# Kernel optimization log

Hardware: AMD Instinct MI355X
Metric: run time of the kernel (lower is better)

## Reference

```python
import jax, jax.numpy as jnp
import numpy as np

B, S, H, E, V, NSTEPS = 8, 128, 512, 512, 32000, 8


def setup_inputs() -> dict:
    key = jax.random.key(0)
    ks = jax.random.split(key, 24)

    def lin(k, fi, fo):
        return (jax.random.normal(k, (fi, fo), jnp.float32) / np.sqrt(fi).astype(np.float32))

    return {
        "input_ids": jax.random.randint(ks[0], (B, S), 0, V),
        "tree_ids": jax.random.randint(ks[1], (B, NSTEPS, 3, S), 0, S),
        "emb": jax.random.normal(ks[2], (V, E), jnp.float32) * 0.02,
        "W_ioux": lin(ks[3], E, 3 * H),
        "W_iouh_r": lin(ks[4], H, 3 * H),
        "b_iouh_r": jnp.zeros((3 * H,), jnp.float32),
        "W_iouh_l": lin(ks[5], H, 3 * H),
        "b_iouh_l": jnp.zeros((3 * H,), jnp.float32),
        "W_fx": lin(ks[6], E, H),
        "W_fh0": lin(ks[7], H, H),
        "b_fh0": jnp.zeros((H,), jnp.float32),
        "W_fh1": lin(ks[8], H, H),
        "b_fh1": jnp.zeros((H,), jnp.float32),
        "W_fh2": lin(ks[9], H, H),
        "b_fh2": jnp.zeros((H,), jnp.float32),
        "W_fh3": lin(ks[10], H, H),
        "b_fh3": jnp.zeros((H,), jnp.float32),
    }


def _scatter_rows(vals, idx):
    # out[b, idx[b, j], k] += vals[b, j, k]  (torch scatter_add_ along dim 1)
    return jax.vmap(lambda v, i: jnp.zeros_like(v).at[i].add(v))(vals, idx)


def _gather_rows(vals, idx):
    # out[b, j, k] = vals[b, idx[b, j], k]  (torch gather along dim 1)
    return jnp.take_along_axis(vals, idx[:, :, None], axis=1)


def _masked_scatter(dest, mask_rows, src):
    # Exact torch masked_scatter_ semantics: flatten mask/src, fill True slots
    # with consecutive elements of flattened src.
    m = jnp.broadcast_to(mask_rows[:, :, None], dest.shape).reshape(-1)
    pos = jnp.clip(jnp.cumsum(m) - 1, 0, None)
    out = jnp.where(m, src.reshape(-1)[pos], dest.reshape(-1))
    return out.reshape(dest.shape)


def reference(input_ids, tree_ids, emb, W_ioux, W_iouh_r, b_iouh_r, W_iouh_l,
              b_iouh_l, W_fx, W_fh0, b_fh0, W_fh1, b_fh1, W_fh2, b_fh2,
              W_fh3, b_fh3):
    x = emb[input_ids]                      # [B, S, E]
    Hs = W_fx.shape[1]
    iou_x = x @ W_ioux                      # [B, S, 3H], loop-invariant
    fx_x = x @ W_fx                         # [B, S, H],  loop-invariant
    h0 = jnp.zeros(x.shape[:2] + (Hs,), x.dtype)
    c0 = jnp.zeros_like(h0)
    steps = jnp.transpose(tree_ids, (1, 0, 2, 3))  # [n_steps, B, 3, S]

    def step(carry, t):
        h, c = carry
        idx_d, idx_r, idx_l = t[:, 0], t[:, 1], t[:, 2]
        iou_hr = h @ W_iouh_r + b_iouh_r
        iou_hl = h @ W_iouh_l + b_iouh_l
        # torch scatter_add_ with an index of width H into a 3H buffer only
        # touches the first H channels -- replicate that exactly.
        scat = _scatter_rows(iou_hr[..., :Hs], idx_r) + _scatter_rows(iou_hl[..., :Hs], idx_l)
        iou = iou_x.at[..., :Hs].add(scat)
        i, o, u = jnp.split(iou, 3, axis=-1)
        i, o, u = jax.nn.sigmoid(i), jax.nn.sigmoid(o), jnp.tanh(u)
        # fh0 and fh1 share idx_r, fh2 and fh3 share idx_l -> fold linearly.
        fh_r = h @ (W_fh0 + W_fh1) + (b_fh0 + b_fh1)
        fh_l = h @ (W_fh2 + W_fh3) + (b_fh2 + b_fh3)
        f = jax.nn.sigmoid(_gather_rows(fx_x, idx_d)
                           + _gather_rows(fh_r, idx_r)
                           + _gather_rows(fh_l, idx_l))
        fc = f * c
        c_full = i * u + _scatter_rows(fc, idx_d)
        h_full = o * jnp.tanh(c_full)
        mask = idx_d != 0
        h_new = _masked_scatter(h, mask, h_full)
        c_new = _masked_scatter(c, mask, c_full)
        return (h_new, c_new), None

    (h, c), _ = jax.lax.scan(step, (h0, c0), steps)
    return h
```

## Files before the change

kernel.cpp:

```cpp
#include <hip/hip_runtime.h>
#include <hip/hip_bf16.h>

#define B_ 8
#define S_ 128
#define H_ 512
#define E_ 512
#define NST 8
#define R_ 1024
#define N2 2048
#define KD 512
#define LDA 72
#define NBLK 512
#define GRP 64

typedef __hip_bfloat16 bf16;
typedef __attribute__((ext_vector_type(8))) short v8s;
typedef __attribute__((ext_vector_type(4))) float v4f;
typedef unsigned long long u64;

__device__ __forceinline__ float sigm(float x){ return 1.0f/(1.0f + expf(-x)); }
__device__ __forceinline__ float load_in(const void* p, long long i, int isb){
    return isb ? __bfloat162float(((const bf16*)p)[i]) : ((const float*)p)[i];
}
__device__ __forceinline__ int idx_read(const int* p, int j, int is64){
    return is64 ? p[2*j] : p[j];
}
__device__ __forceinline__ unsigned short f2b(float v){
    bf16 b = __float2bfloat16(v);
    return *(unsigned short*)&b;
}

__device__ __forceinline__ float2 vload2(const float* p){
    union { u64 u; float2 f; } c;
    c.u = __hip_atomic_load((const u64*)p, __ATOMIC_RELAXED, __HIP_MEMORY_SCOPE_AGENT);
    return c.f;
}
__device__ __forceinline__ void vstore2(float* p, float2 v){
    union { float2 f; u64 u; } c; c.f = v;
    __hip_atomic_store((u64*)p, c.u, __ATOMIC_RELAXED, __HIP_MEMORY_SCOPE_AGENT);
}
__device__ __forceinline__ void vstore1(float* p, float v){
    __hip_atomic_store(p, v, __ATOMIC_RELAXED, __HIP_MEMORY_SCOPE_AGENT);
}
__device__ __forceinline__ void vstore_hb2(unsigned short* p, unsigned short a, unsigned short b){
    unsigned int u = (unsigned)a | ((unsigned)b << 16);
    __hip_atomic_store((unsigned int*)p, u, __ATOMIC_RELAXED, __HIP_MEMORY_SCOPE_AGENT);
}
__device__ __forceinline__ v8s vload16(const unsigned short* p){
    union { u64 u[2]; v8s v; } c;
    c.u[0] = __hip_atomic_load((const u64*)p,     __ATOMIC_RELAXED, __HIP_MEMORY_SCOPE_AGENT);
    c.u[1] = __hip_atomic_load(((const u64*)p)+1, __ATOMIC_RELAXED, __HIP_MEMORY_SCOPE_AGENT);
    return c.v;
}

__device__ __forceinline__ void gsync(int* bar, int gen){
    __syncthreads();
    if (threadIdx.x == 0){
        int g = blockIdx.x >> 6;
        int* ga = bar + 64*(1+g);
        int* gd = bar + 64*(9+g);
        int old = __hip_atomic_fetch_add(ga, 1, __ATOMIC_RELAXED, __HIP_MEMORY_SCOPE_AGENT);
        if (old + 1 == GRP*gen){
            __hip_atomic_fetch_add(bar, GRP, __ATOMIC_RELAXED, __HIP_MEMORY_SCOPE_AGENT);
            while (__hip_atomic_load(bar, __ATOMIC_RELAXED, __HIP_MEMORY_SCOPE_AGENT) < NBLK*gen)
                __builtin_amdgcn_s_sleep(4);
            __hip_atomic_fetch_add(gd, 1, __ATOMIC_RELAXED, __HIP_MEMORY_SCOPE_AGENT);
        } else {
            while (__hip_atomic_load(gd, __ATOMIC_RELAXED, __HIP_MEMORY_SCOPE_AGENT) < gen)
                __builtin_amdgcn_s_sleep(4);
        }
    }
    __syncthreads();
}

__global__ void probe_all(const void* t0, const void* t1, const void* t2, const void* t3,
                          const void* t4, const void* t5, const void* t6, const void* t7,
                          const void* t8, const void* t9, const void* t10, const void* t11,
                          const void* t12, const void* t13, const void* t14,
                          const int* __restrict__ ids, const int* __restrict__ tree,
                          int* __restrict__ flags){
    const void* ts[15] = {t0,t1,t2,t3,t4,t5,t6,t7,t8,t9,t10,t11,t12,t13,t14};
    int bid = blockIdx.x, t = threadIdx.x;
    int bad = 0;
    if (bid < 15){
        if (t < 512){
            unsigned short u = ((const unsigned short*)ts[bid])[t];
            bad = (((u >> 7) & 0xFF) >= 140);
        }
    } else {
        const int* p = (bid == 15) ? ids : tree;
        int n = (bid == 15) ? 1024 : 2048;
        for (int j = t; j < n; j += 1024)
            if (j & 1) bad |= (p[j] != 0);
    }
    unsigned long long bl = __ballot(bad);
    __shared__ int acc[16];
    if ((t & 63) == 0) acc[t >> 6] = (bl != 0ull) ? 1 : 0;
    __syncthreads();
    if (t == 0){
        int any = 0;
        for (int w = 0; w < 16; ++w) any |= acc[w];
        flags[(bid < 15) ? bid : (16 + bid - 15)] = any ? 0 : 1;
    }
}

#define NB2 320
#define GS2 (NB2*512)
__global__ __launch_bounds__(512)
void rank_pack(const void* __restrict__ Wioux, const void* __restrict__ Wfx,
               const void* __restrict__ Wr, const void* __restrict__ Wl,
               const void* __restrict__ W0, const void* __restrict__ W1,
               const void* __restrict__ W2, const void* __restrict__ W3,
               const void* __restrict__ br, const void* __restrict__ bl,
               const void* __restrict__ b0, const void* __restrict__ b1,
               const void* __restrict__ b2, const void* __restrict__ b3,
               const int* __restrict__ ids, const void* __restrict__ emb,
               const int* __restrict__ tree,
               unsigned short* __restrict__ WxT, unsigned short* __restrict__ WcatT,
               float* __restrict__ bcat, unsigned short* __restrict__ xb,
               float* __restrict__ h0,
               int* __restrict__ msk, int* __restrict__ rnk, int* __restrict__ cnt,
               const int* __restrict__ flags, int* __restrict__ bar){
    int bid = blockIdx.x, tid = threadIdx.x;
    int is64 = flags[17];
    if (bid == 0){
        for (int i = tid; i < 64*17; i += 512) bar[i] = 0;
    }
    if (bid < 8){
        int st = bid;
        for (int c = tid; c < R_; c += 512){
            cnt[(0*NST + st)*R_ + c] = 0;
            cnt[(1*NST + st)*R_ + c] = 0;
            cnt[(2*NST + st)*R_ + c] = 0;
        }
        __syncthreads();
        __shared__ int wt[8];
        int runbase = 0;
        for (int ch = 0; ch < 2; ++ch){
            int t = ch*512 + tid;
            int b = t >> 7, s = t & 127;
            int base = (b*NST + st)*3*S_;
            int d0 = idx_read(tree, base + s, is64);
            int rd = (b<<7) + d0;
            int rr = (b<<7) + idx_read(tree, base + S_ + s, is64);
            int rl = (b<<7) + idx_read(tree, base + 2*S_ + s, is64);
            int m = (d0 != 0) ? 1 : 0;
            unsigned long long bal = __ballot(m);
            int lane = tid & 63, wv = tid >> 6;
            if (lane == 0) wt[wv] = __popcll(bal);
            __syncthreads();
            int bp = runbase, tot = 0;
            for (int w = 0; w < wv; ++w) bp += wt[w];
            for (int w = 0; w < 8; ++w) tot += wt[w];
            int rank = bp + __popcll(bal & ((1ull << lane) - 1ull));
            msk[st*R_ + t] = m;
            rnk[st*R_ + t] = m ? rank : 0;
            atomicAdd(&cnt[(0*NST + st)*R_ + rr], 1);
            atomicAdd(&cnt[(1*NST + st)*R_ + rl], 1);
            atomicAdd(&cnt[(2*NST + st)*R_ + rd], 1);
            runbase += tot;
            __syncthreads();
        }
    }
    int gt = bid*512 + tid;
    {
        int f_wx = flags[1], f_wf = flags[6];
        for (int u = gt; u < 131072; u += GS2){
            int n = u >> 6, k0 = (u & 63)*8;
            unsigned short tmp[8];
            #pragma unroll
            for (int i = 0; i < 8; ++i){
                float v = (n < 1536) ? load_in(Wioux, (long long)(k0+i)*1536 + n, f_wx)
                                     : load_in(Wfx,   (long long)(k0+i)*512 + (n-1536), f_wf);
                tmp[i] = f2b(v);
            }
            *(v8s*)&WxT[(size_t)n*KD + k0] = *(v8s*)tmp;
        }
    }
    {
        int fWr=flags[2], fWl=flags[4], fW0=flags[7], fW1=flags[9], fW2=flags[11], fW3=flags[13];
        for (int u = gt; u < 131072; u += GS2){
            int n = u >> 6, k0 = (u & 63)*8;
            unsigned short tmp[8];
            #pragma unroll
            for (int i = 0; i < 8; ++i){
                long long k = k0 + i;
                float v;
                if      (n <  512) v = load_in(Wr, k*1536 + n, fWr);
                else if (n < 1024) v = load_in(Wl, k*1536 + (n-512), fWl);
                else if (n < 1536) { int c = n-1024; v = load_in(W0, k*512+c, fW0) + load_in(W1, k*512+c, fW1); }
                else               { int c = n-1536; v = load_in(W2, k*512+c, fW2) + load_in(W3, k*512+c, fW3); }
                tmp[i] = f2b(v);
            }
            *(v8s*)&WcatT[(size_t)n*KD + k0] = *(v8s*)tmp;
        }
    }
    {
        int fbr=flags[3], fbl=flags[5], fb0=flags[8], fb1=flags[10], fb2=flags[12], fb3=flags[14];
        for (int n = gt; n < 2048; n += GS2){
            float v;
            if      (n <  512) v = load_in(br, n, fbr);
            else if (n < 1024) v = load_in(bl, n-512, fbl);
            else if (n < 1536) v = load_in(b0, n-1024, fb0) + load_in(b1, n-1024, fb1);
            else               v = load_in(b2, n-1536, fb2) + load_in(b3, n-1536, fb3);
            bcat[n] = v;
        }
    }
    {
        int f_emb = flags[0], i64i = flags[16];
        for (int u = gt; u < 65536; u += GS2){
            int r = u >> 6, c0 = (u & 63)*8;
            long long base = (long long)idx_read(ids, r, i64i)*E_ + c0;
            unsigned short tmp[8];
            #pragma unroll
            for (int i = 0; i < 8; ++i) tmp[i] = f2b(load_in(emb, base + i, f_emb));
            *(v8s*)&xb[(size_t)r*KD + c0] = *(v8s*)tmp;
        }
    }
    for (int u = gt; u < 262144; u += GS2)
        ((float4*)h0)[u] = make_float4(0.f,0.f,0.f,0.f);
}

__global__ void csr_scan(const int* __restrict__ cnt, int* __restrict__ off,
                         int* __restrict__ cur){
    int st = blockIdx.x, a = blockIdx.y;
    int t = threadIdx.x;
    int base = (a*NST + st)*R_;
    __shared__ int sh[R_];
    int v = cnt[base + t];
    sh[t] = v;
    __syncthreads();
    for (int d = 1; d < R_; d <<= 1){
        int x = (t >= d) ? sh[t - d] : 0;
        __syncthreads();
        sh[t] += x;
        __syncthreads();
    }
    int excl = sh[t] - v;
    off[base + t] = excl;
    cur[base + t] = excl;
}

__global__ __launch_bounds__(512)
void csr_fill(const int* __restrict__ tree, int* __restrict__ cur,
              int* __restrict__ ent, const int* __restrict__ flags){
    int is64 = flags[17];
    int st = blockIdx.x;
    for (int ch = 0; ch < 2; ++ch){
        int t = ch*512 + threadIdx.x;
        int b = t >> 7, s = t & 127;
        int base = (b*NST + st)*3*S_;
        int rd = (b<<7) + idx_read(tree, base + s, is64);
        int rr = (b<<7) + idx_read(tree, base + S_ + s, is64);
        int rl = (b<<7) + idx_read(tree, base + 2*S_ + s, is64);
        int p0 = atomicAdd(&cur[(0*NST + st)*R_ + rr], 1);
        ent[(0*NST + st)*R_ + p0] = t;
        int p1 = atomicAdd(&cur[(1*NST + st)*R_ + rl], 1);
        ent[(1*NST + st)*R_ + p1] = t;
        int p2 = atomicAdd(&cur[(2*NST + st)*R_ + rd], 1);
        ent[(2*NST + st)*R_ + p2] = t | (rr << 10) | (rl << 20);
    }
}

__device__ __forceinline__ void gemm_phase(const unsigned short* __restrict__ A,
               const unsigned short* __restrict__ BT,
               const float* __restrict__ bias,
               float* __restrict__ C,
               short* __restrict__ As, short* __restrict__ Bs)
{
    int bid = blockIdx.x;
    int bn = (bid & 7)*4 + ((bid >> 3) & 3);
    int bm = bid >> 5;
    int tid = threadIdx.x;
    int lane = tid & 63, wave = tid >> 6;
    int wm = wave & 1, wn = wave >> 1;
    int lm = lane & 15, quad = lane >> 4;
    v4f acc[2][2];
    #pragma unroll
    for (int i=0;i<2;++i)
        #pragma unroll
        for (int j=0;j<2;++j) acc[i][j] = (v4f)0.0f;

    int srow = tid >> 3, sg = (tid & 7)*8;
    const unsigned short* Ab = A  + (size_t)(bm*64)*KD;
    const unsigned short* Bb = BT + (size_t)(bn*64)*KD;
    v8s pa[2], pb[2];
    #pragma unroll
    for (int j=0;j<2;++j){
        pa[j] = vload16(Ab + (size_t)(j*32+srow)*KD + sg);
        pb[j] = *(const v8s*)(Bb + (size_t)(j*32+srow)*KD + sg);
    }
    for (int k0 = 0; k0 < KD; k0 += 64){
        #pragma unroll
        for (int j=0;j<2;++j){
            *(v8s*)&As[(j*32+srow)*LDA + sg] = pa[j];
            *(v8s*)&Bs[(j*32+srow)*LDA + sg] = pb[j];
        }
        __syncthreads();
        int k1 = k0 + 64;
        if (k1 < KD){
            #pragma unroll
            for (int j=0;j<2;++j){
                pa[j] = vload16(Ab + (size_t)(j*32+srow)*KD + k1 + sg);
                pb[j] = *(const v8s*)(Bb + (size_t)(j*32+srow)*KD + k1 + sg);
            }
        }
        #pragma unroll
        for (int kk = 0; kk < 64; kk += 32){
            v8s af[2], bf[2];
            #pragma unroll
            for (int i=0;i<2;++i){
                af[i] = *(const v8s*)&As[(wm*32 + i*16 + lm)*LDA + kk + quad*8];
                bf[i] = *(const v8s*)&Bs[(wn*32 + i*16 + lm)*LDA + kk + quad*8];
            }
            #pragma unroll
            for (int i=0;i<2;++i)
                #pragma unroll
                for (int j=0;j<2;++j)
                    acc[i][j] = __builtin_amdgcn_mfma_f32_16x16x32_bf16(af[i], bf[j], acc[i][j], 0, 0, 0);
        }
        __syncthreads();
    }
    #pragma unroll
    for (int j=0;j<2;++j){
        int n = bn*64 + wn*32 + j*16 + lm;
        float bv = bias ? bias[n] : 0.0f;
        #pragma unroll
        for (int i=0;i<2;++i){
            int m0 = bm*64 + wm*32 + i*16 + quad*4;
            #pragma unroll
            for (int rg = 0; rg < 4; ++rg)
                vstore1(&C[(size_t)(m0+rg)*N2 + n], acc[i][j][rg] + bv);
        }
    }
}

__device__ __forceinline__ void epi_phase(const float* __restrict__ XO,
              const float* __restrict__ T, int tstr,
              const float* __restrict__ hc, const float* __restrict__ cc,
              float* __restrict__ hn, float* __restrict__ cn,
              unsigned short* __restrict__ hb, float* __restrict__ out,
              const int* __restrict__ msk, const int* __restrict__ rnk,
              const int* __restrict__ cnt, const int* __restrict__ off,
              const int* __restrict__ ent, int st, int last)
{
    int tid = threadIdx.x;
    int c0 = tid*2;
    #pragma unroll
    for (int rr2 = 0; rr2 < 2; ++rr2){
        int r = blockIdx.x*2 + rr2;
        if (!msk[st*R_ + r]){
            float2 hv = vload2(&hc[(size_t)r*H_ + c0]);
            if (last){
                out[(size_t)r*H_ + c0]     = hv.x;
                out[(size_t)r*H_ + c0 + 1] = hv.y;
            } else {
                vstore2(&hn[(size_t)r*H_ + c0], hv);
                float2 cv = vload2(&cc[(size_t)r*H_ + c0]);
                vstore2(&cn[(size_t)r*H_ + c0], cv);
                vstore_hb2(&hb[(size_t)r*KD + c0], f2b(hv.x), f2b(hv.y));
            }
            continue;
        }
        int j = rnk[st*R_ + r];
        int bR = off[(0*NST+st)*R_ + j], dR = cnt[(0*NST+st)*R_ + j];
        int bL = off[(1*NST+st)*R_ + j], dL = cnt[(1*NST+st)*R_ + j];
        int bD = off[(2*NST+st)*R_ + j], dD = cnt[(2*NST+st)*R_ + j];
        const int* eR = ent + (0*NST+st)*R_ + bR;
        const int* eL = ent + (1*NST+st)*R_ + bL;
        const int* eD = ent + (2*NST+st)*R_ + bD;
        const float* xo = XO + (size_t)j*N2;
        float scv0 = 0.f, scv1 = 0.f;
        for (int e = 0; e < dR; ++e){
            float2 t = vload2(&T[(size_t)eR[e]*tstr + c0]);
            scv0 += t.x; scv1 += t.y;
        }
        for (int e = 0; e < dL; ++e){
            float2 t = vload2(&T[(size_t)eL[e]*tstr + 512 + c0]);
            scv0 += t.x; scv1 += t.y;
        }
        float2 fx = vload2(&xo[1536 + c0]);
        float csc0 = 0.f, csc1 = 0.f;
        for (int e = 0; e < dD; ++e){
            int pk = eD[e];
            int s  = pk & 1023, ra = (pk >> 10) & 1023, rb = (pk >> 20) & 1023;
            float2 ta = vload2(&T[(size_t)ra*tstr + 1024 + c0]);
            float2 tb = vload2(&T[(size_t)rb*tstr + 1536 + c0]);
            float2 cv = vload2(&cc[(size_t)s*H_ + c0]);
            float f0 = sigm(fx.x + ta.x + tb.x);
            float f1 = sigm(fx.y + ta.y + tb.y);
            csc0 += f0 * cv.x;
            csc1 += f1 * cv.y;
        }
        float2 xi = vload2(&xo[c0]);
        float2 xq = vload2(&xo[512 + c0]);
        float2 xu = vload2(&xo[1024 + c0]);
        float ig0 = sigm(xi.x + scv0), ig1 = sigm(xi.y + scv1);
        float og0 = sigm(xq.x), og1 = sigm(xq.y);
        float ug0 = tanhf(xu.x), ug1 = tanhf(xu.y);
        float cf0 = ig0*ug0 + csc0, cf1 = ig1*ug1 + csc1;
        float hf0 = og0 * tanhf(cf0), hf1 = og1 * tanhf(cf1);
        if (last){
            out[(size_t)r*H_ + c0]     = hf0;
            out[(size_t)r*H_ + c0 + 1] = hf1;
        } else {
            vstore2(&hn[(size_t)r*H_ + c0], make_float2(hf0, hf1));
            vstore2(&cn[(size_t)r*H_ + c0], make_float2(cf0, cf1));
            vstore_hb2(&hb[(size_t)r*KD + c0], f2b(hf0), f2b(hf1));
        }
    }
}

__global__ __launch_bounds__(256, 2)
void chain_all(const unsigned short* __restrict__ xb,
               const unsigned short* __restrict__ WxT,
               const unsigned short* __restrict__ WcatT,
               const float* __restrict__ bcat,
               float* __restrict__ XO, float* __restrict__ T,
               float* __restrict__ h0, float* __restrict__ c0,
               float* __restrict__ h1, float* __restrict__ c1,
               unsigned short* __restrict__ hb, float* __restrict__ out,
               const int* __restrict__ msk, const int* __restrict__ rnk,
               const int* __restrict__ cnt, const int* __restrict__ off,
               const int* __restrict__ ent, int* bar)
{
    __shared__ short As[64*LDA];
    __shared__ short Bs[64*LDA];
    int gen = 0;

    gemm_phase(xb, WxT, (const float*)nullptr, XO, As, Bs);
    gsync(bar, ++gen);
    epi_phase(XO, bcat, 0, h0, c0, h1, c1, hb, out, msk, rnk, cnt, off, ent, 0, 0);
    gsync(bar, ++gen);

    for (int st = 1; st < NST; ++st){
        const float* hcp = (st & 1) ? h1 : h0;
        const float* ccp = (st & 1) ? c1 : c0;
        float* hnp = (st & 1) ? h0 : h1;
        float* cnp = (st & 1) ? c0 : c1;
        gemm_phase(hb, WcatT, bcat, T, As, Bs);
        gsync(bar, ++gen);
        epi_phase(XO, T, N2, hcp, ccp, hnp, cnp, hb, out,
                  msk, rnk, cnt, off, ent, st, (st == NST-1) ? 1 : 0);
        if (st < NST-1) gsync(bar, ++gen);
    }
}

extern "C" void kernel_launch(void* const* d_in, const int* in_sizes, int n_in,
                              void* d_out, int out_size, void* d_ws, size_t ws_size,
                              hipStream_t stream) {
    const int* input_ids = (const int*)d_in[0];
    const int* tree      = (const int*)d_in[1];

    char* wp = (char*)d_ws;
    auto alloc = [&](size_t bytes) -> void* {
        void* q = (void*)wp;
        wp += (bytes + 255) & ~(size_t)255;
        return q;
    };
    float*          XO     = (float*)alloc((size_t)R_*N2*4);
    float*          T      = (float*)alloc((size_t)R_*N2*4);
    float*          h0     = (float*)alloc((size_t)R_*H_*4);
    float*          c0     = (float*)alloc((size_t)R_*H_*4);
    float*          h1     = (float*)alloc((size_t)R_*H_*4);
    float*          c1     = (float*)alloc((size_t)R_*H_*4);
    unsigned short* WxT    = (unsigned short*)alloc((size_t)N2*KD*2);
    unsigned short* WcatT  = (unsigned short*)alloc((size_t)N2*KD*2);
    float*          bcat   = (float*)alloc((size_t)N2*4);
    unsigned short* xb     = (unsigned short*)alloc((size_t)R_*KD*2);
    unsigned short* hb     = (unsigned short*)alloc((size_t)R_*KD*2);
    int*            msk    = (int*)alloc((size_t)NST*R_*4);
    int*            rnk    = (int*)alloc((size_t)NST*R_*4);
    int*            cnt    = (int*)alloc((size_t)3*NST*R_*4);
    int*            off    = (int*)alloc((size_t)3*NST*R_*4);
    int*            cur    = (int*)alloc((size_t)3*NST*R_*4);
    int*            ent    = (int*)alloc((size_t)3*NST*R_*4);
    int*            flags  = (int*)alloc(256);
    int*            bar    = (int*)alloc(8192);
    float*          out    = (float*)d_out;

    hipLaunchKernelGGL(probe_all, dim3(17), dim3(1024), 0, stream,
                       d_in[2], d_in[3], d_in[4], d_in[5], d_in[6], d_in[7], d_in[8],
                       d_in[9], d_in[10], d_in[11], d_in[12], d_in[13], d_in[14],
                       d_in[15], d_in[16], input_ids, tree, flags);
    hipLaunchKernelGGL(rank_pack, dim3(NB2), dim3(512), 0, stream,
                       d_in[3], d_in[8],
                       d_in[4], d_in[6], d_in[9], d_in[11], d_in[13], d_in[15],
                       d_in[5], d_in[7], d_in[10], d_in[12], d_in[14], d_in[16],
                       input_ids, d_in[2], tree,
                       WxT, WcatT, bcat, xb, h0, msk, rnk, cnt, flags, bar);
    hipLaunchKernelGGL(csr_scan, dim3(NST, 3), dim3(1024), 0, stream, cnt, off, cur);
    hipLaunchKernelGGL(csr_fill, dim3(NST), dim3(512), 0, stream, tree, cur, ent, flags);

    hipLaunchKernelGGL(chain_all, dim3(NBLK), dim3(256), 0, stream,
                       xb, WxT, WcatT, bcat, XO, T, h0, c0, h1, c1, hb, out,
                       msk, rnk, cnt, off, ent, bar);
}
```

Before: 306.0 us.

## Double block threads: split-K GEMM across wave groups, one column per thread in epilogue

Raises the persistent kernel's block size from 256 to 512 threads. In the GEMM phase the two wave groups each take half of K and combine partial sums through shared memory. In the epilogue each thread handles one column instead of two, with the gather loops unrolled for more loads in flight, and bf16 pairs for the h buffer assembled with a lane shuffle. The aim is more parallelism per block in the latency-bound recurrent steps, at the cost of a shared-memory reduction, an extra barrier, and narrower loads.

```diff
diff --git a/kernel.cpp b/kernel.cpp
--- a/kernel.cpp
+++ b/kernel.cpp
@@ -30,14 +30,8 @@
     return *(unsigned short*)&b;
 }
 
-__device__ __forceinline__ float2 vload2(const float* p){
-    union { u64 u; float2 f; } c;
-    c.u = __hip_atomic_load((const u64*)p, __ATOMIC_RELAXED, __HIP_MEMORY_SCOPE_AGENT);
-    return c.f;
-}
-__device__ __forceinline__ void vstore2(float* p, float2 v){
-    union { float2 f; u64 u; } c; c.f = v;
-    __hip_atomic_store((u64*)p, c.u, __ATOMIC_RELAXED, __HIP_MEMORY_SCOPE_AGENT);
+__device__ __forceinline__ float vload1f(const float* p){
+    return __hip_atomic_load(p, __ATOMIC_RELAXED, __HIP_MEMORY_SCOPE_AGENT);
 }
 __device__ __forceinline__ void vstore1(float* p, float v){
     __hip_atomic_store(p, v, __ATOMIC_RELAXED, __HIP_MEMORY_SCOPE_AGENT);
@@ -266,31 +260,36 @@
                const unsigned short* __restrict__ BT,
                const float* __restrict__ bias,
                float* __restrict__ C,
-               short* __restrict__ As, short* __restrict__ Bs)
+               short* __restrict__ SMEM)
 {
     int bid = blockIdx.x;
     int bn = (bid & 7)*4 + ((bid >> 3) & 3);
     int bm = bid >> 5;
     int tid = threadIdx.x;
     int lane = tid & 63, wave = tid >> 6;
-    int wm = wave & 1, wn = wave >> 1;
+    int grp = wave >> 2, w4 = wave & 3;
+    int wm = w4 & 1, wn = w4 >> 1;
     int lm = lane & 15, quad = lane >> 4;
+    short* As = SMEM + grp*(2*64*LDA);
+    short* Bs = As + 64*LDA;
     v4f acc[2][2];
     #pragma unroll
     for (int i=0;i<2;++i)
         #pragma unroll
         for (int j=0;j<2;++j) acc[i][j] = (v4f)0.0f;
 
-    int srow = tid >> 3, sg = (tid & 7)*8;
-    const unsigned short* Ab = A  + (size_t)(bm*64)*KD;
-    const unsigned short* Bb = BT + (size_t)(bn*64)*KD;
+    int t = tid & 255;
+    int srow = t >> 3, sg = (t & 7)*8;
+    int kb = grp*256;
+    const unsigned short* Ab = A  + (size_t)(bm*64)*KD + kb;
+    const unsigned short* Bb = BT + (size_t)(bn*64)*KD + kb;
     v8s pa[2], pb[2];
     #pragma unroll
     for (int j=0;j<2;++j){
         pa[j] = vload16(Ab + (size_t)(j*32+srow)*KD + sg);
         pb[j] = *(const v8s*)(Bb + (size_t)(j*32+srow)*KD + sg);
     }
-    for (int k0 = 0; k0 < KD; k0 += 64){
+    for (int k0 = 0; k0 < 256; k0 += 64){
         #pragma unroll
         for (int j=0;j<2;++j){
             *(v8s*)&As[(j*32+srow)*LDA + sg] = pa[j];
@@ -298,7 +297,7 @@
         }
         __syncthreads();
         int k1 = k0 + 64;
-        if (k1 < KD){
+        if (k1 < 256){
             #pragma unroll
             for (int j=0;j<2;++j){
                 pa[j] = vload16(Ab + (size_t)(j*32+srow)*KD + k1 + sg);
@@ -321,16 +320,31 @@
         }
         __syncthreads();
     }
-    #pragma unroll
-    for (int j=0;j<2;++j){
-        int n = bn*64 + wn*32 + j*16 + lm;
-        float bv = bias ? bias[n] : 0.0f;
+    float* Red = (float*)SMEM;
+    if (grp){
         #pragma unroll
-        for (int i=0;i<2;++i){
-            int m0 = bm*64 + wm*32 + i*16 + quad*4;
-            #pragma unroll
-            for (int rg = 0; rg < 4; ++rg)
-                vstore1(&C[(size_t)(m0+rg)*N2 + n], acc[i][j][rg] + bv);
+        for (int i=0;i<2;++i)
+            #pragma unroll
+            for (int j=0;j<2;++j)
+                #pragma unroll
+                for (int rg=0;rg<4;++rg)
+                    Red[(wm*32 + i*16 + quad*4 + rg)*64 + (wn*32 + j*16 + lm)] = acc[i][j][rg];
+    }
+    __syncthreads();
+    if (!grp){
+        #pragma unroll
+        for (int j=0;j<2;++j){
+            int n = bn*64 + wn*32 + j*16 + lm;
+            float bv = bias ? bias[n] : 0.0f;
+            #pragma unroll
+            for (int i=0;i<2;++i){
+                int m0 = bm*64 + wm*32 + i*16 + quad*4;
+                #pragma unroll
+                for (int rg = 0; rg < 4; ++rg){
+                    float v = acc[i][j][rg] + Red[(wm*32 + i*16 + quad*4 + rg)*64 + (wn*32 + j*16 + lm)] + bv;
+                    vstore1(&C[(size_t)(m0+rg)*N2 + n], v);
+                }
+            }
         }
     }
 }
@@ -344,21 +358,20 @@
               const int* __restrict__ cnt, const int* __restrict__ off,
               const int* __restrict__ ent, int st, int last)
 {
-    int tid = threadIdx.x;
-    int c0 = tid*2;
+    int c = threadIdx.x;
     #pragma unroll
     for (int rr2 = 0; rr2 < 2; ++rr2){
         int r = blockIdx.x*2 + rr2;
         if (!msk[st*R_ + r]){
-            float2 hv = vload2(&hc[(size_t)r*H_ + c0]);
+            float hv = vload1f(&hc[(size_t)r*H_ + c]);
             if (last){
-                out[(size_t)r*H_ + c0]     = hv.x;
-                out[(size_t)r*H_ + c0 + 1] = hv.y;
+                out[(size_t)r*H_ + c] = hv;
             } else {
-                vstore2(&hn[(size_t)r*H_ + c0], hv);
-                float2 cv = vload2(&cc[(size_t)r*H_ + c0]);
-                vstore2(&cn[(size_t)r*H_ + c0], cv);
-                vstore_hb2(&hb[(size_t)r*KD + c0], f2b(hv.x), f2b(hv.y));
+                vstore1(&hn[(size_t)r*H_ + c], hv);
+                vstore1(&cn[(size_t)r*H_ + c], vload1f(&cc[(size_t)r*H_ + c]));
+                unsigned v16 = f2b(hv);
+                unsigned o16 = __shfl_down((int)v16, 1);
+                if (!(c & 1)) vstore_hb2(&hb[(size_t)r*KD + c], (unsigned short)v16, (unsigned short)o16);
             }
             continue;
         }
@@ -370,48 +383,74 @@
         const int* eL = ent + (1*NST+st)*R_ + bL;
         const int* eD = ent + (2*NST+st)*R_ + bD;
         const float* xo = XO + (size_t)j*N2;
-        float scv0 = 0.f, scv1 = 0.f;
-        for (int e = 0; e < dR; ++e){
-            float2 t = vload2(&T[(size_t)eR[e]*tstr + c0]);
-            scv0 += t.x; scv1 += t.y;
-        }
-        for (int e = 0; e < dL; ++e){
-            float2 t = vload2(&T[(size_t)eL[e]*tstr + 512 + c0]);
-            scv0 += t.x; scv1 += t.y;
-        }
-        float2 fx = vload2(&xo[1536 + c0]);
-        float csc0 = 0.f, csc1 = 0.f;
-        for (int e = 0; e < dD; ++e){
-            int pk = eD[e];
-            int s  = pk & 1023, ra = (pk >> 10) & 1023, rb = (pk >> 20) & 1023;
-            float2 ta = vload2(&T[(size_t)ra*tstr + 1024 + c0]);
-            float2 tb = vload2(&T[(size_t)rb*tstr + 1536 + c0]);
-            float2 cv = vload2(&cc[(size_t)s*H_ + c0]);
-            float f0 = sigm(fx.x + ta.x + tb.x);
-            float f1 = sigm(fx.y + ta.y + tb.y);
-            csc0 += f0 * cv.x;
-            csc1 += f1 * cv.y;
-        }
-        float2 xi = vload2(&xo[c0]);
-        float2 xq = vload2(&xo[512 + c0]);
-        float2 xu = vload2(&xo[1024 + c0]);
-        float ig0 = sigm(xi.x + scv0), ig1 = sigm(xi.y + scv1);
-        float og0 = sigm(xq.x), og1 = sigm(xq.y);
-        float ug0 = tanhf(xu.x), ug1 = tanhf(xu.y);
-        float cf0 = ig0*ug0 + csc0, cf1 = ig1*ug1 + csc1;
-        float hf0 = og0 * tanhf(cf0), hf1 = og1 * tanhf(cf1);
+        float scv = 0.f;
+        {
+            int e = 0;
+            for (; e + 4 <= dR; e += 4){
+                int a0=eR[e], a1=eR[e+1], a2=eR[e+2], a3=eR[e+3];
+                float t0 = vload1f(&T[(size_t)a0*tstr + c]);
+                float t1 = vload1f(&T[(size_t)a1*tstr + c]);
+                float t2 = vload1f(&T[(size_t)a2*tstr + c]);
+                float t3 = vload1f(&T[(size_t)a3*tstr + c]);
+                scv += (t0 + t1) + (t2 + t3);
+            }
+            for (; e < dR; ++e) scv += vload1f(&T[(size_t)eR[e]*tstr + c]);
+        }
+        {
+            int e = 0;
+            for (; e + 4 <= dL; e += 4){
+                int a0=eL[e], a1=eL[e+1], a2=eL[e+2], a3=eL[e+3];
+                float t0 = vload1f(&T[(size_t)a0*tstr + 512 + c]);
+                float t1 = vload1f(&T[(size_t)a1*tstr + 512 + c]);
+                float t2 = vload1f(&T[(size_t)a2*tstr + 512 + c]);
+                float t3 = vload1f(&T[(size_t)a3*tstr + 512 + c]);
+                scv += (t0 + t1) + (t2 + t3);
+            }
+            for (; e < dL; ++e) scv += vload1f(&T[(size_t)eL[e]*tstr + 512 + c]);
+        }
+        float fxv = vload1f(&xo[1536 + c]);
+        float csc = 0.f;
+        {
+            int e = 0;
+            for (; e + 2 <= dD; e += 2){
+                int p0 = eD[e], p1 = eD[e+1];
+                int s0 = p0 & 1023, ra0 = (p0 >> 10) & 1023, rb0 = (p0 >> 20) & 1023;
+                int s1 = p1 & 1023, ra1 = (p1 >> 10) & 1023, rb1 = (p1 >> 20) & 1023;
+                float ta0 = vload1f(&T[(size_t)ra0*tstr + 1024 + c]);
+                float tb0 = vload1f(&T[(size_t)rb0*tstr + 1536 + c]);
+                float cv0 = vload1f(&cc[(size_t)s0*H_ + c]);
+                float ta1 = vload1f(&T[(size_t)ra1*tstr + 1024 + c]);
+                float tb1 = vload1f(&T[(size_t)rb1*tstr + 1536 + c]);
+                float cv1 = vload1f(&cc[(size_t)s1*H_ + c]);
+                csc += sigm(fxv + ta0 + tb0) * cv0 + sigm(fxv + ta1 + tb1) * cv1;
+            }
+            for (; e < dD; ++e){
+                int pk = eD[e];
+                int s  = pk & 1023, ra = (pk >> 10) & 1023, rb = (pk >> 20) & 1023;
+                float ta = vload1f(&T[(size_t)ra*tstr + 1024 + c]);
+                float tb = vload1f(&T[(size_t)rb*tstr + 1536 + c]);
+                float cv = vload1f(&cc[(size_t)s*H_ + c]);
+                csc += sigm(fxv + ta + tb) * cv;
+            }
+        }
+        float ig = sigm(vload1f(&xo[c]) + scv);
+        float og = sigm(vload1f(&xo[512 + c]));
+        float ug = tanhf(vload1f(&xo[1024 + c]));
+        float cf = ig*ug + csc;
+        float hf = og * tanhf(cf);
         if (last){
-            out[(size_t)r*H_ + c0]     = hf0;
-            out[(size_t)r*H_ + c0 + 1] = hf1;
+            out[(size_t)r*H_ + c] = hf;
         } else {
-            vstore2(&hn[(size_t)r*H_ + c0], make_float2(hf0, hf1));
-            vstore2(&cn[(size_t)r*H_ + c0], make_float2(cf0, cf1));
-            vstore_hb2(&hb[(size_t)r*KD + c0], f2b(hf0), f2b(hf1));
-        }
-    }
-}
-
-__global__ __launch_bounds__(256, 2)
+            vstore1(&hn[(size_t)r*H_ + c], hf);
+            vstore1(&cn[(size_t)r*H_ + c], cf);
+            unsigned v16 = f2b(hf);
+            unsigned o16 = __shfl_down((int)v16, 1);
+            if (!(c & 1)) vstore_hb2(&hb[(size_t)r*KD + c], (unsigned short)v16, (unsigned short)o16);
+        }
+    }
+}
+
+__global__ __launch_bounds__(512, 4)
 void chain_all(const unsigned short* __restrict__ xb,
                const unsigned short* __restrict__ WxT,
                const unsigned short* __restrict__ WcatT,
@@ -424,11 +463,10 @@
                const int* __restrict__ cnt, const int* __restrict__ off,
                const int* __restrict__ ent, int* bar)
 {
-    __shared__ short As[64*LDA];
-    __shared__ short Bs[64*LDA];
+    __shared__ short SMEM[4*64*LDA];
     int gen = 0;
 
-    gemm_phase(xb, WxT, (const float*)nullptr, XO, As, Bs);
+    gemm_phase(xb, WxT, (const float*)nullptr, XO, SMEM);
     gsync(bar, ++gen);
     epi_phase(XO, bcat, 0, h0, c0, h1, c1, hb, out, msk, rnk, cnt, off, ent, 0, 0);
     gsync(bar, ++gen);
@@ -438,7 +476,7 @@
         const float* ccp = (st & 1) ? c1 : c0;
         float* hnp = (st & 1) ? h0 : h1;
         float* cnp = (st & 1) ? c0 : c1;
-        gemm_phase(hb, WcatT, bcat, T, As, Bs);
+        gemm_phase(hb, WcatT, bcat, T, SMEM);
         gsync(bar, ++gen);
         epi_phase(XO, T, N2, hcp, ccp, hnp, cnp, hb, out,
                   msk, rnk, cnt, off, ent, st, (st == NST-1) ? 1 : 0);
@@ -492,7 +530,7 @@
     hipLaunchKernelGGL(csr_scan, dim3(NST, 3), dim3(1024), 0, stream, cnt, off, cur);
     hipLaunchKernelGGL(csr_fill, dim3(NST), dim3(512), 0, stream, tree, cur, ent, flags);
 
-    hipLaunchKernelGGL(chain_all, dim3(NBLK), dim3(256), 0, stream,
+    hipLaunchKernelGGL(chain_all, dim3(NBLK), dim3(512), 0, stream,
                        xb, WxT, WcatT, bcat, XO, T, h0, c0, h1, c1, hb, out,
                        msk, rnk, cnt, off, ent, bar);
 }
```

After: 295.5 us. -3.4%, faster.
